# Kernel optimization log

Hardware: AMD Instinct MI355X
Metric: run time of the kernel (lower is better)

The kernel has to match this reference:

```python
import jax, jax.numpy as jnp
import numpy as np


def setup_inputs() -> dict:
    key = jax.random.key(0)
    k1, k2 = jax.random.split(key)
    n, t, c, l = 32, 64, 256, 64
    query = jax.random.normal(k1, (n, t, c, l), dtype=jnp.float32)
    key_t = jax.random.normal(k2, (t, n, c), dtype=jnp.float32)
    return {"query": query, "key": key_t}


def reference(query, key):
    # scores[n,l] = sum_{t,c} query[n,t,c,l] * key[t,n,c]
    scores = jnp.einsum('ntcl,tnc->nl', query, key)
    scores = jax.nn.softmax(scores, axis=1)
    # out[t,n,c] = sum_l query[n,t,c,l] * scores[n,l]
    out = jnp.einsum('ntcl,nl->tnc', query, scores)
    return out
```

## Files before the change

kernel.cpp:

```cpp
#include <hip/hip_runtime.h>

#define N 32
#define T 64
#define C 256
#define L 64
#define TC (T * C)
#define BLK_PER_N 64

__global__ __launch_bounds__(256, 8) void scores_partial_kernel(
    const float* __restrict__ q, const float* __restrict__ k,
    float* __restrict__ partial) {
  const int t    = blockIdx.x;
  const int n    = blockIdx.y;
  const int tid  = threadIdx.x;
  const int lane = tid & 63;
  const int wave = tid >> 6;
  const int sub  = lane >> 4;
  const int lq   = lane & 15;
  const int g    = wave * 4 + sub;

  __shared__ float ks[C];
  ks[tid] = k[t * (N * C) + n * C + tid];
  __syncthreads();

  const float* qnt = q + ((size_t)n * T + t) * (C * L);

  float4 acc = make_float4(0.f, 0.f, 0.f, 0.f);
  #pragma unroll 8
  for (int c = g; c < C; c += 16) {
    const float4 qv = *reinterpret_cast<const float4*>(qnt + (size_t)c * L + lq * 4);
    const float kv = ks[c];
    acc.x = fmaf(qv.x, kv, acc.x);
    acc.y = fmaf(qv.y, kv, acc.y);
    acc.z = fmaf(qv.z, kv, acc.z);
    acc.w = fmaf(qv.w, kv, acc.w);
  }

  acc.x += __shfl_xor(acc.x, 16); acc.y += __shfl_xor(acc.y, 16);
  acc.z += __shfl_xor(acc.z, 16); acc.w += __shfl_xor(acc.w, 16);
  acc.x += __shfl_xor(acc.x, 32); acc.y += __shfl_xor(acc.y, 32);
  acc.z += __shfl_xor(acc.z, 32); acc.w += __shfl_xor(acc.w, 32);

  __shared__ float sdata[4 * L];
  if (lane < 16) {
    sdata[wave * L + lq * 4 + 0] = acc.x;
    sdata[wave * L + lq * 4 + 1] = acc.y;
    sdata[wave * L + lq * 4 + 2] = acc.z;
    sdata[wave * L + lq * 4 + 3] = acc.w;
  }
  __syncthreads();
  if (tid < L) {
    const float s = sdata[tid] + sdata[L + tid] + sdata[2 * L + tid] + sdata[3 * L + tid];
    partial[(size_t)t * (N * L) + n * L + tid] = s;
  }
}

__global__ __launch_bounds__(256, 8) void out_kernel(
    const float* __restrict__ q, const float* __restrict__ partial,
    float* __restrict__ out) {
  const int t    = blockIdx.x;
  const int n    = blockIdx.y;
  const int tid  = threadIdx.x;
  const int lane = tid & 63;
  const int wave = tid >> 6;

  __shared__ float sred[4 * L];
  __shared__ float probs[L];
  {
    float s = 0.f;
    #pragma unroll 4
    for (int b = wave * 16; b < wave * 16 + 16; ++b)
      s += partial[(size_t)b * (N * L) + n * L + lane];
    sred[wave * L + lane] = s;
  }
  __syncthreads();
  if (tid < L) {
    float s = sred[tid] + sred[L + tid] + sred[2 * L + tid] + sred[3 * L + tid];
    float m = s;
    #pragma unroll
    for (int off = 32; off > 0; off >>= 1) m = fmaxf(m, __shfl_xor(m, off));
    const float e = __expf(s - m);
    float sum = e;
    #pragma unroll
    for (int off = 32; off > 0; off >>= 1) sum += __shfl_xor(sum, off);
    probs[tid] = e / sum;
  }
  __syncthreads();

  const int sub = lane >> 4;
  const int lq  = lane & 15;
  const int g   = wave * 4 + sub;

  const float4 pv = *reinterpret_cast<const float4*>(&probs[lq * 4]);
  const float* qnt = q + ((size_t)n * T + t) * (C * L);

  #pragma unroll 8
  for (int c = g; c < C; c += 16) {
    const float4 qv = *reinterpret_cast<const float4*>(qnt + (size_t)c * L + lq * 4);
    float d = qv.x * pv.x + qv.y * pv.y + qv.z * pv.z + qv.w * pv.w;
    d += __shfl_xor(d, 1);
    d += __shfl_xor(d, 2);
    d += __shfl_xor(d, 4);
    d += __shfl_xor(d, 8);
    if (lq == 0) {
      __builtin_nontemporal_store(d, &out[t * (N * C) + n * C + c]);
    }
  }
}

extern "C" void kernel_launch(void* const* d_in, const int* in_sizes, int n_in,
                              void* d_out, int out_size, void* d_ws, size_t ws_size,
                              hipStream_t stream) {
  const float* q = (const float*)d_in[0];
  const float* k = (const float*)d_in[1];
  float* out = (float*)d_out;
  float* partial = (float*)d_ws;

  dim3 grid(BLK_PER_N, N);
  scores_partial_kernel<<<grid, 256, 0, stream>>>(q, k, partial);
  out_kernel<<<grid, 256, 0, stream>>>(q, partial, out);
}
```

Baseline: 212.4 us.

## Fuse score and output passes into one kernel with grid barrier and register reuse

Merges the two kernels into a single persistent launch in which each block handles two time steps. A global atomic spin barrier separates the score reduction from the softmax and output stage. The first time step's query tile stays in registers across the barrier so it is not re-read, cutting total query traffic. This relies on all 1024 blocks being co-resident, otherwise the barrier deadlocks, and it lowers occupancy and adds a memset plus barrier spin cost.

```diff
diff --git a/kernel.cpp b/kernel.cpp
--- a/kernel.cpp
+++ b/kernel.cpp
@@ -4,32 +4,54 @@
 #define T 64
 #define C 256
 #define L 64
-#define TC (T * C)
-#define BLK_PER_N 64
+#define CHUNKS 32
+#define GRID_BLOCKS (CHUNKS * N)
+#define PARTIAL_ELEMS (CHUNKS * N * L)
 
-__global__ __launch_bounds__(256, 8) void scores_partial_kernel(
+__global__ __launch_bounds__(256, 4) void fused_kernel(
     const float* __restrict__ q, const float* __restrict__ k,
-    float* __restrict__ partial) {
-  const int t    = blockIdx.x;
-  const int n    = blockIdx.y;
-  const int tid  = threadIdx.x;
-  const int lane = tid & 63;
-  const int wave = tid >> 6;
-  const int sub  = lane >> 4;
-  const int lq   = lane & 15;
-  const int g    = wave * 4 + sub;
+    float* __restrict__ partial, unsigned int* __restrict__ bar,
+    float* __restrict__ out) {
+  const int chunk = blockIdx.x;
+  const int n     = blockIdx.y;
+  const int t0    = chunk * 2;
+  const int tid   = threadIdx.x;
+  const int lane  = tid & 63;
+  const int wave  = tid >> 6;
+  const int sub   = lane >> 4;
+  const int lq    = lane & 15;
+  const int g     = wave * 4 + sub;
 
-  __shared__ float ks[C];
-  ks[tid] = k[t * (N * C) + n * C + tid];
+  __shared__ float ks[2 * C];
+  __shared__ float sdata[4 * L];
+  __shared__ float probs[L];
+
+  ks[tid]       = k[t0 * (N * C) + n * C + tid];
+  ks[tid + C]   = k[(t0 + 1) * (N * C) + n * C + tid];
   __syncthreads();
 
-  const float* qnt = q + ((size_t)n * T + t) * (C * L);
+  const float* q0 = q + ((size_t)n * T + t0) * (C * L);
+  const float* q1 = q0 + (size_t)(C * L);
 
+  float4 hold[16];
+  #pragma unroll
+  for (int j = 0; j < 16; ++j) {
+    const int c = g + j * 16;
+    hold[j] = *reinterpret_cast<const float4*>(q0 + (size_t)c * L + lq * 4);
+  }
   float4 acc = make_float4(0.f, 0.f, 0.f, 0.f);
-  #pragma unroll 8
+  #pragma unroll
+  for (int j = 0; j < 16; ++j) {
+    const float kv = ks[g + j * 16];
+    acc.x = fmaf(hold[j].x, kv, acc.x);
+    acc.y = fmaf(hold[j].y, kv, acc.y);
+    acc.z = fmaf(hold[j].z, kv, acc.z);
+    acc.w = fmaf(hold[j].w, kv, acc.w);
+  }
+  #pragma unroll 4
   for (int c = g; c < C; c += 16) {
-    const float4 qv = *reinterpret_cast<const float4*>(qnt + (size_t)c * L + lq * 4);
-    const float kv = ks[c];
+    const float4 qv = *reinterpret_cast<const float4*>(q1 + (size_t)c * L + lq * 4);
+    const float kv = ks[C + c];
     acc.x = fmaf(qv.x, kv, acc.x);
     acc.y = fmaf(qv.y, kv, acc.y);
     acc.z = fmaf(qv.z, kv, acc.z);
@@ -41,7 +63,6 @@
   acc.x += __shfl_xor(acc.x, 32); acc.y += __shfl_xor(acc.y, 32);
   acc.z += __shfl_xor(acc.z, 32); acc.w += __shfl_xor(acc.w, 32);
 
-  __shared__ float sdata[4 * L];
   if (lane < 16) {
     sdata[wave * L + lq * 4 + 0] = acc.x;
     sdata[wave * L + lq * 4 + 1] = acc.y;
@@ -51,31 +72,31 @@
   __syncthreads();
   if (tid < L) {
     const float s = sdata[tid] + sdata[L + tid] + sdata[2 * L + tid] + sdata[3 * L + tid];
-    partial[(size_t)t * (N * L) + n * L + tid] = s;
+    partial[(size_t)chunk * (N * L) + n * L + tid] = s;
   }
-}
+  __syncthreads();
 
-__global__ __launch_bounds__(256, 8) void out_kernel(
-    const float* __restrict__ q, const float* __restrict__ partial,
-    float* __restrict__ out) {
-  const int t    = blockIdx.x;
-  const int n    = blockIdx.y;
-  const int tid  = threadIdx.x;
-  const int lane = tid & 63;
-  const int wave = tid >> 6;
+  if (tid == 0) {
+    __threadfence();
+    atomicAdd(bar, 1u);
+    while (__hip_atomic_load(bar, __ATOMIC_ACQUIRE, __HIP_MEMORY_SCOPE_AGENT)
+           < (unsigned)GRID_BLOCKS) {
+      __builtin_amdgcn_s_sleep(8);
+    }
+    __threadfence();
+  }
+  __syncthreads();
 
-  __shared__ float sred[4 * L];
-  __shared__ float probs[L];
   {
     float s = 0.f;
-    #pragma unroll 4
-    for (int b = wave * 16; b < wave * 16 + 16; ++b)
+    #pragma unroll
+    for (int b = wave * 8; b < wave * 8 + 8; ++b)
       s += partial[(size_t)b * (N * L) + n * L + lane];
-    sred[wave * L + lane] = s;
+    sdata[wave * L + lane] = s;
   }
   __syncthreads();
   if (tid < L) {
-    float s = sred[tid] + sred[L + tid] + sred[2 * L + tid] + sred[3 * L + tid];
+    float s = sdata[tid] + sdata[L + tid] + sdata[2 * L + tid] + sdata[3 * L + tid];
     float m = s;
     #pragma unroll
     for (int off = 32; off > 0; off >>= 1) m = fmaxf(m, __shfl_xor(m, off));
@@ -87,24 +108,28 @@
   }
   __syncthreads();
 
-  const int sub = lane >> 4;
-  const int lq  = lane & 15;
-  const int g   = wave * 4 + sub;
+  const float4 pv = *reinterpret_cast<const float4*>(&probs[lq * 4]);
 
-  const float4 pv = *reinterpret_cast<const float4*>(&probs[lq * 4]);
-  const float* qnt = q + ((size_t)n * T + t) * (C * L);
-
-  #pragma unroll 8
+  #pragma unroll
+  for (int j = 0; j < 16; ++j) {
+    float d = hold[j].x * pv.x + hold[j].y * pv.y + hold[j].z * pv.z + hold[j].w * pv.w;
+    d += __shfl_xor(d, 1);
+    d += __shfl_xor(d, 2);
+    d += __shfl_xor(d, 4);
+    d += __shfl_xor(d, 8);
+    if (lq == 0)
+      __builtin_nontemporal_store(d, &out[t0 * (N * C) + n * C + (g + j * 16)]);
+  }
+  #pragma unroll 4
   for (int c = g; c < C; c += 16) {
-    const float4 qv = *reinterpret_cast<const float4*>(qnt + (size_t)c * L + lq * 4);
+    const float4 qv = *reinterpret_cast<const float4*>(q1 + (size_t)c * L + lq * 4);
     float d = qv.x * pv.x + qv.y * pv.y + qv.z * pv.z + qv.w * pv.w;
     d += __shfl_xor(d, 1);
     d += __shfl_xor(d, 2);
     d += __shfl_xor(d, 4);
     d += __shfl_xor(d, 8);
-    if (lq == 0) {
-      __builtin_nontemporal_store(d, &out[t * (N * C) + n * C + c]);
-    }
+    if (lq == 0)
+      __builtin_nontemporal_store(d, &out[(t0 + 1) * (N * C) + n * C + c]);
   }
 }
 
@@ -115,8 +140,10 @@
   const float* k = (const float*)d_in[1];
   float* out = (float*)d_out;
   float* partial = (float*)d_ws;
+  unsigned int* bar = (unsigned int*)((char*)d_ws + (size_t)PARTIAL_ELEMS * 4);
 
-  dim3 grid(BLK_PER_N, N);
-  scores_partial_kernel<<<grid, 256, 0, stream>>>(q, k, partial);
-  out_kernel<<<grid, 256, 0, stream>>>(q, partial, out);
+  hipMemsetAsync((void*)bar, 0, sizeof(unsigned int), stream);
+
+  dim3 grid(CHUNKS, N);
+  fused_kernel<<<grid, 256, 0, stream>>>(q, k, partial, bar, out);
 }
```

After: 357.8 us. 68.4% more time.
